# Optimization experiments

Hardware: AMD Instinct MI355X
Metric: run time of the kernel (lower is better)

Reference implementation:

```python
import jax, jax.numpy as jnp
import numpy as np

B, S, HID, HEADS, INTER = 64, 512, 40, 4, 20
DH = HID // HEADS  # 10
EPS = 1e-5


def layer_norm(x, g, b):
    mu = jnp.mean(x, axis=-1, keepdims=True)
    var = jnp.mean(jnp.square(x - mu), axis=-1, keepdims=True)
    return (x - mu) * jax.lax.rsqrt(var + EPS) * g + b


def setup_inputs() -> dict:
    key = jax.random.key(0)
    ks = jax.random.split(key, 16)
    s = 0.05
    return {
        "hidden_states": jax.random.normal(ks[0], (B, S, HID), jnp.float32),
        "ln1_g": jnp.ones((HID,), jnp.float32),
        "ln1_b": jnp.zeros((HID,), jnp.float32),
        "Wq": jax.random.normal(ks[1], (HID, HID), jnp.float32) * s,
        "bq": jnp.zeros((HID,), jnp.float32),
        "Wk": jax.random.normal(ks[2], (HID, HID), jnp.float32) * s,
        "bk": jnp.zeros((HID,), jnp.float32),
        "Wv": jax.random.normal(ks[3], (HID, HID), jnp.float32) * s,
        "bv": jnp.zeros((HID,), jnp.float32),
        "Wo": jax.random.normal(ks[4], (HID, HID), jnp.float32) * s,
        "bo": jnp.zeros((HID,), jnp.float32),
        "ln2_g": jnp.ones((HID,), jnp.float32),
        "ln2_b": jnp.zeros((HID,), jnp.float32),
        "W1": jax.random.normal(ks[5], (HID, INTER), jnp.float32) * s,
        "b1": jnp.zeros((INTER,), jnp.float32),
        "W2": jax.random.normal(ks[6], (INTER, HID), jnp.float32) * s,
        "b2": jnp.zeros((HID,), jnp.float32),
    }


def reference(hidden_states, ln1_g, ln1_b, Wq, bq, Wk, bk, Wv, bv, Wo, bo,
              ln2_g, ln2_b, W1, b1, W2, b2):
    x = hidden_states
    # --- self-attention (pre-LN) ---
    h = layer_norm(x, ln1_g, ln1_b)
    q = (h @ Wq + bq).reshape(B, S, HEADS, DH)
    k = (h @ Wk + bk).reshape(B, S, HEADS, DH)
    v = (h @ Wv + bv).reshape(B, S, HEADS, DH)
    # scores: [B, H, S, S]
    scores = jnp.einsum('bqhd,bkhd->bhqk', q, k) / jnp.sqrt(jnp.float32(DH))
    probs = jax.nn.softmax(scores, axis=-1)
    ctx = jnp.einsum('bhqk,bkhd->bqhd', probs, v).reshape(B, S, HID)
    attn_out = ctx @ Wo + bo + x
    # --- FFN (pre-LN) ---
    h2 = layer_norm(attn_out, ln2_g, ln2_b)
    inter = jax.nn.gelu(h2 @ W1 + b1, approximate=False)
    out = inter @ W2 + b2 + attn_out
    return out
```

## Files before the change

kernel.cpp:

```cpp
#include <hip/hip_runtime.h>
#include <stdint.h>

#define EPSF 1e-5f

typedef __attribute__((ext_vector_type(8)))  short bh8;
typedef __attribute__((ext_vector_type(16))) float fx16;
typedef __attribute__((ext_vector_type(4)))  int   i32x4;

__device__ __forceinline__ int cvtpk(float a, float b) {
    int r;
    asm("v_cvt_pk_bf16_f32 %0, %1, %2" : "=v"(r) : "v"(a), "v"(b));
    return r;
}
__device__ __forceinline__ float fastrcp(float x) {
    float r;
    asm("v_rcp_f32 %0, %1" : "=v"(r) : "v"(x));
    return r;
}

__global__ __launch_bounds__(512) void k_qkv_attn(
    const float* __restrict__ x, const float* __restrict__ g, const float* __restrict__ be,
    const float* __restrict__ Wq, const float* __restrict__ bq,
    const float* __restrict__ Wk, const float* __restrict__ bk,
    const float* __restrict__ Wv, const float* __restrict__ bv,
    float* __restrict__ ctx)
{
    __shared__ __align__(16) char smem[83968];

    const int tid = threadIdx.x;
    const int bh = blockIdx.x;
    const int b  = bh >> 2;
    const int h  = bh & 3;
    const int lane = tid & 63;
    const int wavei = tid >> 6;

    float* sX = (float*)smem;
    {
        const float4* xb = (const float4*)(x + (size_t)b * 512 * 40);
        for (int idx = tid; idx < 5120; idx += 512) {
            float4 u = xb[idx];
            int fl = idx * 4;
            int r = fl / 40, c = fl - r * 40;
            sX[r * 41 + c] = u.x; sX[r * 41 + c + 1] = u.y;
            sX[r * 41 + c + 2] = u.z; sX[r * 41 + c + 3] = u.w;
        }
    }
    __syncthreads();

    float s1 = 0.f, s2 = 0.f;
#pragma unroll 8
    for (int i = 0; i < 40; i++) { float v = sX[tid * 41 + i]; s1 += v; s2 += v * v; }
    const float mu = s1 * 0.025f;
    const float rs = rsqrtf(s2 * 0.025f - mu * mu + EPSF);

    float hrow[40];
#pragma unroll 4
    for (int i = 0; i < 40; i++)
        hrow[i] = (sX[tid * 41 + i] - mu) * rs * g[i] + be[i];

    float aq[10], ak[10], av[10];
#pragma unroll
    for (int c = 0; c < 10; c++) {
        aq[c] = bq[h * 10 + c]; ak[c] = bk[h * 10 + c]; av[c] = bv[h * 10 + c];
    }
#pragma unroll 2
    for (int i = 0; i < 40; i++) {
        const float hi = hrow[i];
        const float* wq = Wq + i * 40 + h * 10;
        const float* wk = Wk + i * 40 + h * 10;
        const float* wv = Wv + i * 40 + h * 10;
#pragma unroll
        for (int c = 0; c < 10; c++) {
            aq[c] += hi * wq[c]; ak[c] += hi * wk[c]; av[c] += hi * wv[c];
        }
    }
    const float cs = 1.4426950408889634f / 3.1622776601683795f;
#pragma unroll
    for (int c = 0; c < 10; c++) aq[c] *= cs;

    __syncthreads();

    char* sK  = smem;
    char* sVT = smem + 24576;
    char* sQ  = smem + 41216;
    {
        int p0 = cvtpk(ak[0], ak[1]), p1 = cvtpk(ak[2], ak[3]);
        int p2 = cvtpk(ak[4], ak[5]), p3 = cvtpk(ak[6], ak[7]);
        int p4 = cvtpk(ak[8], ak[9]);
        i32x4* kd = (i32x4*)(sK + tid * 48);
        kd[0] = (i32x4){p0, p1, p2, p3};
        kd[1] = (i32x4){p4, 0, 0, 0};
    }
    {
        int p0 = cvtpk(aq[0], aq[1]), p1 = cvtpk(aq[2], aq[3]);
        int p2 = cvtpk(aq[4], aq[5]), p3 = cvtpk(aq[6], aq[7]);
        int p4 = cvtpk(aq[8], aq[9]);
        i32x4* qd = (i32x4*)(sQ + tid * 32);
        qd[0] = (i32x4){p0, p1, p2, p3};
        qd[1] = (i32x4){p4, 0, 0, 0};
    }
    {
        int p0 = cvtpk(av[0], av[1]), p1 = cvtpk(av[2], av[3]);
        int p2 = cvtpk(av[4], av[5]), p3 = cvtpk(av[6], av[7]);
        int p4 = cvtpk(av[8], av[9]);
        unsigned short* vb = (unsigned short*)sVT + tid;
        vb[0 * 520] = (unsigned short)(p0 & 0xffff);
        vb[1 * 520] = (unsigned short)((unsigned)p0 >> 16);
        vb[2 * 520] = (unsigned short)(p1 & 0xffff);
        vb[3 * 520] = (unsigned short)((unsigned)p1 >> 16);
        vb[4 * 520] = (unsigned short)(p2 & 0xffff);
        vb[5 * 520] = (unsigned short)((unsigned)p2 >> 16);
        vb[6 * 520] = (unsigned short)(p3 & 0xffff);
        vb[7 * 520] = (unsigned short)((unsigned)p3 >> 16);
        vb[8 * 520] = (unsigned short)(p4 & 0xffff);
        vb[9 * 520] = (unsigned short)((unsigned)p4 >> 16);
        vb[10 * 520] = 0x3F80;
        vb[11 * 520] = 0; vb[12 * 520] = 0; vb[13 * 520] = 0;
        vb[14 * 520] = 0; vb[15 * 520] = 0;
    }
    __syncthreads();

    const int krow = lane & 31, khalf = lane >> 5;
    const int vrow = lane & 15;
    const bool vzero = (lane & 16) != 0;

    bh8 qf0 = *(const bh8*)(sQ + (size_t)(wavei * 64 + (lane & 31)) * 32 + (lane >> 5) * 16);
    bh8 qf1 = *(const bh8*)(sQ + (size_t)(wavei * 64 + 32 + (lane & 31)) * 32 + (lane >> 5) * 16);

    fx16 acc0 = (fx16)(0.0f), acc1 = (fx16)(0.0f);

    for (int kt = 0; kt < 16; ++kt) {
        bh8 kf  = *(const bh8*)(sK + (kt * 32 + krow) * 48 + khalf * 16);
        bh8 vf0 = *(const bh8*)(sVT + vrow * 1040 + kt * 64 + khalf * 16);
        bh8 vf1 = *(const bh8*)(sVT + vrow * 1040 + kt * 64 + 32 + khalf * 16);
        if (vzero) { vf0 = (bh8)(short)0; vf1 = (bh8)(short)0; }
#pragma unroll
        for (int qt = 0; qt < 2; ++qt) {
            fx16 s = __builtin_amdgcn_mfma_f32_32x32x16_bf16(
                kf, qt ? qf1 : qf0, (fx16)(0.0f), 0, 0, 0);
            float e[16];
#pragma unroll
            for (int r = 0; r < 16; ++r) e[r] = __builtin_amdgcn_exp2f(s[r]);
            int c0 = cvtpk(e[0], e[1]),   c1 = cvtpk(e[2], e[3]);
            int c2 = cvtpk(e[4], e[5]),   c3 = cvtpk(e[6], e[7]);
            int c4 = cvtpk(e[8], e[9]),   c5 = cvtpk(e[10], e[11]);
            int c6 = cvtpk(e[12], e[13]), c7 = cvtpk(e[14], e[15]);
            asm("v_permlane32_swap_b32 %0, %1" : "+v"(c0), "+v"(c2));
            asm("v_permlane32_swap_b32 %0, %1" : "+v"(c1), "+v"(c3));
            asm("v_permlane32_swap_b32 %0, %1" : "+v"(c4), "+v"(c6));
            asm("v_permlane32_swap_b32 %0, %1" : "+v"(c5), "+v"(c7));
            union { i32x4 i; bh8 h; } lo, hi;
            lo.i = (i32x4){c0, c1, c2, c3};
            hi.i = (i32x4){c4, c5, c6, c7};
            if (qt == 0) {
                acc0 = __builtin_amdgcn_mfma_f32_32x32x16_bf16(lo.h, vf0, acc0, 0, 0, 0);
                acc0 = __builtin_amdgcn_mfma_f32_32x32x16_bf16(hi.h, vf1, acc0, 0, 0, 0);
            } else {
                acc1 = __builtin_amdgcn_mfma_f32_32x32x16_bf16(lo.h, vf0, acc1, 0, 0, 0);
                acc1 = __builtin_amdgcn_mfma_f32_32x32x16_bf16(hi.h, vf1, acc1, 0, 0, 0);
            }
        }
    }

    const int d = lane & 31;
    const int qb = wavei * 64;
#pragma unroll
    for (int qt = 0; qt < 2; ++qt) {
        fx16 A = qt ? acc1 : acc0;
#pragma unroll
        for (int r = 0; r < 16; ++r) {
            float v = A[r];
            float ls = __shfl(v, (lane & 32) | 10, 64);
            float o = v * fastrcp(ls);
            if (d < 10) {
                int q = qb + qt * 32 + (r & 3) + 8 * (r >> 2) + 4 * (lane >> 5);
                ctx[((size_t)bh * 512 + q) * 10 + d] = o;
            }
        }
    }
}

__global__ __launch_bounds__(256) void k_out_ffn(
    const float* __restrict__ ctx, const float* __restrict__ x,
    const float* __restrict__ Wo, const float* __restrict__ bo,
    const float* __restrict__ g2, const float* __restrict__ bt2,
    const float* __restrict__ W1, const float* __restrict__ b1,
    const float* __restrict__ W2, const float* __restrict__ b2,
    float* __restrict__ out)
{
    __shared__ float sWo[40][48];
    __shared__ float sW1[40][32];
    __shared__ float sW2[20][48];
    __shared__ float sBo[40], sG2[40], sBt2[40], sB1[20], sB2[40];
    __shared__ float sCtx[64][41];
    __shared__ float sH[64][41];
    __shared__ float sIt[64][21];
    __shared__ float sSum[64][4], sSum2[64][4];

    const int tid = threadIdx.x;
    for (int idx = tid; idx < 1600; idx += 256) {
        int i = idx / 40, j = idx % 40;
        sWo[i][(j / 10) * 12 + (j % 10)] = Wo[idx];
    }
    for (int idx = tid; idx < 800; idx += 256) {
        {
            int i = idx / 20, j = idx % 20;
            sW1[i][(j / 5) * 8 + (j % 5)] = W1[idx];
        }
        {
            int i = idx / 40, j = idx % 40;
            sW2[i][(j / 10) * 12 + (j % 10)] = W2[idx];
        }
    }
    if (tid < 40) { sBo[tid] = bo[tid]; sG2[tid] = g2[tid]; sBt2[tid] = bt2[tid]; sB2[tid] = b2[tid]; }
    if (tid < 20) sB1[tid] = b1[tid];

    const int row0 = blockIdx.x * 64;
    const int b = row0 >> 9, s0 = row0 & 511;

    for (int idx = tid; idx < 640; idx += 256) {
        const int hh = idx / 160, f = idx - hh * 160;
        float4 u = *(const float4*)(ctx + ((size_t)((b * 4 + hh) * 512 + s0)) * 10 + f * 4);
        const int fo = f * 4;
        float e[4] = {u.x, u.y, u.z, u.w};
#pragma unroll
        for (int t = 0; t < 4; t++) {
            const int fe = fo + t;
            const int r = fe / 10, c = fe - r * 10;
            sCtx[r][hh * 10 + c] = e[t];
        }
    }
    const float4* xblk = (const float4*)(x + (size_t)blockIdx.x * 64 * 40);
    for (int idx = tid; idx < 640; idx += 256) {
        float4 w = xblk[idx];
        int fl = idx * 4;
        int r = fl / 40, c = fl - r * 40;
        sH[r][c] = w.x; sH[r][c + 1] = w.y; sH[r][c + 2] = w.z; sH[r][c + 3] = w.w;
    }
    __syncthreads();

    const int lane = tid & 63;
    const int wv = tid >> 6;
    const int j0 = wv * 10;

    float acc[10];
#pragma unroll
    for (int j = 0; j < 10; j++) acc[j] = sBo[j0 + j] + sH[lane][j0 + j];
#pragma unroll 8
    for (int i = 0; i < 40; i++) {
        const float ci = sCtx[lane][i];
        const float4* wrow = (const float4*)&sWo[i][wv * 12];
        float4 w0 = wrow[0], w1 = wrow[1], w2 = wrow[2];
        acc[0] += ci * w0.x; acc[1] += ci * w0.y; acc[2] += ci * w0.z; acc[3] += ci * w0.w;
        acc[4] += ci * w1.x; acc[5] += ci * w1.y; acc[6] += ci * w1.z; acc[7] += ci * w1.w;
        acc[8] += ci * w2.x; acc[9] += ci * w2.y;
    }
    {
        float s1 = 0.f, s2 = 0.f;
#pragma unroll
        for (int j = 0; j < 10; j++) { s1 += acc[j]; s2 += acc[j] * acc[j]; }
        sSum[lane][wv] = s1; sSum2[lane][wv] = s2;
    }
    __syncthreads();
    const float mu = (sSum[lane][0] + sSum[lane][1] + sSum[lane][2] + sSum[lane][3]) * 0.025f;
    const float ex2 = (sSum2[lane][0] + sSum2[lane][1] + sSum2[lane][2] + sSum2[lane][3]) * 0.025f;
    const float rs = rsqrtf(ex2 - mu * mu + EPSF);
#pragma unroll
    for (int j = 0; j < 10; j++)
        sH[lane][j0 + j] = (acc[j] - mu) * rs * sG2[j0 + j] + sBt2[j0 + j];
    __syncthreads();

    const int f0 = wv * 5;
    float it[5];
#pragma unroll
    for (int j = 0; j < 5; j++) it[j] = sB1[f0 + j];
#pragma unroll 8
    for (int i = 0; i < 40; i++) {
        const float hi = sH[lane][i];
        const float4* wrow = (const float4*)&sW1[i][wv * 8];
        float4 w0 = wrow[0], w1 = wrow[1];
        it[0] += hi * w0.x; it[1] += hi * w0.y; it[2] += hi * w0.z; it[3] += hi * w0.w;
        it[4] += hi * w1.x;
    }
#pragma unroll
    for (int j = 0; j < 5; j++) {
        float t = it[j];
        sIt[lane][f0 + j] = 0.5f * t * (1.0f + erff(t * 0.70710678118654752f));
    }
    __syncthreads();

    float o[10];
#pragma unroll
    for (int j = 0; j < 10; j++) o[j] = acc[j] + sB2[j0 + j];
#pragma unroll 4
    for (int i = 0; i < 20; i++) {
        const float ii = sIt[lane][i];
        const float4* wrow = (const float4*)&sW2[i][wv * 12];
        float4 w0 = wrow[0], w1 = wrow[1], w2 = wrow[2];
        o[0] += ii * w0.x; o[1] += ii * w0.y; o[2] += ii * w0.z; o[3] += ii * w0.w;
        o[4] += ii * w1.x; o[5] += ii * w1.y; o[6] += ii * w1.z; o[7] += ii * w1.w;
        o[8] += ii * w2.x; o[9] += ii * w2.y;
    }
#pragma unroll
    for (int j = 0; j < 10; j++) sCtx[lane][j0 + j] = o[j];
    __syncthreads();

    float4* oblk = (float4*)(out + (size_t)blockIdx.x * 64 * 40);
    for (int idx = tid; idx < 640; idx += 256) {
        int fl = idx * 4;
        int r = fl / 40, c = fl - r * 40;
        float4 u;
        u.x = sCtx[r][c]; u.y = sCtx[r][c + 1]; u.z = sCtx[r][c + 2]; u.w = sCtx[r][c + 3];
        oblk[idx] = u;
    }
}

extern "C" void kernel_launch(void* const* d_in, const int* in_sizes, int n_in,
                              void* d_out, int out_size, void* d_ws, size_t ws_size,
                              hipStream_t stream)
{
    const float* x   = (const float*)d_in[0];
    const float* g1  = (const float*)d_in[1];
    const float* be1 = (const float*)d_in[2];
    const float* Wq  = (const float*)d_in[3];
    const float* bq  = (const float*)d_in[4];
    const float* Wk  = (const float*)d_in[5];
    const float* bk  = (const float*)d_in[6];
    const float* Wv  = (const float*)d_in[7];
    const float* bv  = (const float*)d_in[8];
    const float* Wo  = (const float*)d_in[9];
    const float* bo  = (const float*)d_in[10];
    const float* g2  = (const float*)d_in[11];
    const float* bt2 = (const float*)d_in[12];
    const float* W1  = (const float*)d_in[13];
    const float* b1  = (const float*)d_in[14];
    const float* W2  = (const float*)d_in[15];
    const float* b2  = (const float*)d_in[16];

    float* ctx = (float*)d_ws;

    k_qkv_attn<<<256, 512, 0, stream>>>(x, g1, be1, Wq, bq, Wk, bk, Wv, bv, ctx);
    k_out_ffn<<<512, 256, 0, stream>>>(ctx, x, Wo, bo, g2, bt2, W1, b1, W2, b2,
                                       (float*)d_out);
}
```

Measured before the change: 129.3 us.

## Store ctx token-major and compute out-proj/FFN per row in one wave

The attention kernel now writes context in [B,S,HID] layout with heads interleaved, so the second kernel can load it with contiguous float4 reads. The out-projection/LN2/FFN kernel is reshaped from 4 waves splitting columns to a single 64-thread wave where each thread owns a full row. This removes the cross-wave LayerNorm reduction, several barriers and the shared-memory weight staging; weights are read directly from global memory as uniform loads. The cost is high register pressure (40+40+20 accumulators per thread) and much lower occupancy per block, since only 512 single-wave blocks are launched.

New measurement: 152.5 us. +18.0%, slower.

```diff
diff --git a/kernel.cpp b/kernel.cpp
--- a/kernel.cpp
+++ b/kernel.cpp
@@ -174,13 +174,13 @@
             float o = v * fastrcp(ls);
             if (d < 10) {
                 int q = qb + qt * 32 + (r & 3) + 8 * (r >> 2) + 4 * (lane >> 5);
-                ctx[((size_t)bh * 512 + q) * 10 + d] = o;
+                ctx[((size_t)b * 512 + q) * 40 + h * 10 + d] = o;
             }
         }
     }
 }
 
-__global__ __launch_bounds__(256) void k_out_ffn(
+__global__ __launch_bounds__(64) void k_out_ffn(
     const float* __restrict__ ctx, const float* __restrict__ x,
     const float* __restrict__ Wo, const float* __restrict__ bo,
     const float* __restrict__ g2, const float* __restrict__ bt2,
@@ -188,129 +188,81 @@
     const float* __restrict__ W2, const float* __restrict__ b2,
     float* __restrict__ out)
 {
-    __shared__ float sWo[40][48];
-    __shared__ float sW1[40][32];
-    __shared__ float sW2[20][48];
-    __shared__ float sBo[40], sG2[40], sBt2[40], sB1[20], sB2[40];
-    __shared__ float sCtx[64][41];
-    __shared__ float sH[64][41];
-    __shared__ float sIt[64][21];
-    __shared__ float sSum[64][4], sSum2[64][4];
+    __shared__ float sX[64][41];
+    __shared__ float sC[64][41];
 
     const int tid = threadIdx.x;
-    for (int idx = tid; idx < 1600; idx += 256) {
-        int i = idx / 40, j = idx % 40;
-        sWo[i][(j / 10) * 12 + (j % 10)] = Wo[idx];
-    }
-    for (int idx = tid; idx < 800; idx += 256) {
-        {
-            int i = idx / 20, j = idx % 20;
-            sW1[i][(j / 5) * 8 + (j % 5)] = W1[idx];
-        }
-        {
-            int i = idx / 40, j = idx % 40;
-            sW2[i][(j / 10) * 12 + (j % 10)] = W2[idx];
-        }
-    }
-    if (tid < 40) { sBo[tid] = bo[tid]; sG2[tid] = g2[tid]; sBt2[tid] = bt2[tid]; sB2[tid] = b2[tid]; }
-    if (tid < 20) sB1[tid] = b1[tid];
-
-    const int row0 = blockIdx.x * 64;
-    const int b = row0 >> 9, s0 = row0 & 511;
-
-    for (int idx = tid; idx < 640; idx += 256) {
-        const int hh = idx / 160, f = idx - hh * 160;
-        float4 u = *(const float4*)(ctx + ((size_t)((b * 4 + hh) * 512 + s0)) * 10 + f * 4);
-        const int fo = f * 4;
-        float e[4] = {u.x, u.y, u.z, u.w};
-#pragma unroll
-        for (int t = 0; t < 4; t++) {
-            const int fe = fo + t;
-            const int r = fe / 10, c = fe - r * 10;
-            sCtx[r][hh * 10 + c] = e[t];
-        }
-    }
     const float4* xblk = (const float4*)(x + (size_t)blockIdx.x * 64 * 40);
-    for (int idx = tid; idx < 640; idx += 256) {
-        float4 w = xblk[idx];
+    const float4* cblk = (const float4*)(ctx + (size_t)blockIdx.x * 64 * 40);
+    for (int idx = tid; idx < 640; idx += 64) {
+        float4 u = xblk[idx];
+        float4 v = cblk[idx];
         int fl = idx * 4;
         int r = fl / 40, c = fl - r * 40;
-        sH[r][c] = w.x; sH[r][c + 1] = w.y; sH[r][c + 2] = w.z; sH[r][c + 3] = w.w;
-    }
-    __syncthreads();
-
-    const int lane = tid & 63;
-    const int wv = tid >> 6;
-    const int j0 = wv * 10;
-
-    float acc[10];
-#pragma unroll
-    for (int j = 0; j < 10; j++) acc[j] = sBo[j0 + j] + sH[lane][j0 + j];
-#pragma unroll 8
+        sX[r][c] = u.x; sX[r][c + 1] = u.y; sX[r][c + 2] = u.z; sX[r][c + 3] = u.w;
+        sC[r][c] = v.x; sC[r][c + 1] = v.y; sC[r][c + 2] = v.z; sC[r][c + 3] = v.w;
+    }
+    __syncthreads();
+
+    float acc[40];
+#pragma unroll 8
+    for (int c = 0; c < 40; c++) acc[c] = sX[tid][c] + bo[c];
+#pragma unroll 2
     for (int i = 0; i < 40; i++) {
-        const float ci = sCtx[lane][i];
-        const float4* wrow = (const float4*)&sWo[i][wv * 12];
-        float4 w0 = wrow[0], w1 = wrow[1], w2 = wrow[2];
-        acc[0] += ci * w0.x; acc[1] += ci * w0.y; acc[2] += ci * w0.z; acc[3] += ci * w0.w;
-        acc[4] += ci * w1.x; acc[5] += ci * w1.y; acc[6] += ci * w1.z; acc[7] += ci * w1.w;
-        acc[8] += ci * w2.x; acc[9] += ci * w2.y;
-    }
-    {
-        float s1 = 0.f, s2 = 0.f;
-#pragma unroll
-        for (int j = 0; j < 10; j++) { s1 += acc[j]; s2 += acc[j] * acc[j]; }
-        sSum[lane][wv] = s1; sSum2[lane][wv] = s2;
-    }
-    __syncthreads();
-    const float mu = (sSum[lane][0] + sSum[lane][1] + sSum[lane][2] + sSum[lane][3]) * 0.025f;
-    const float ex2 = (sSum2[lane][0] + sSum2[lane][1] + sSum2[lane][2] + sSum2[lane][3]) * 0.025f;
-    const float rs = rsqrtf(ex2 - mu * mu + EPSF);
-#pragma unroll
-    for (int j = 0; j < 10; j++)
-        sH[lane][j0 + j] = (acc[j] - mu) * rs * sG2[j0 + j] + sBt2[j0 + j];
-    __syncthreads();
-
-    const int f0 = wv * 5;
-    float it[5];
-#pragma unroll
-    for (int j = 0; j < 5; j++) it[j] = sB1[f0 + j];
-#pragma unroll 8
+        const float ci = sC[tid][i];
+        const float* wp = Wo + i * 40;
+#pragma unroll
+        for (int c = 0; c < 40; c++) acc[c] += ci * wp[c];
+    }
+
+    float s1 = 0.f, s2 = 0.f;
+#pragma unroll 8
+    for (int c = 0; c < 40; c++) { s1 += acc[c]; s2 += acc[c] * acc[c]; }
+    const float mu = s1 * 0.025f;
+    const float rs = rsqrtf(s2 * 0.025f - mu * mu + EPSF);
+
+    float h2[40];
+#pragma unroll 4
+    for (int c = 0; c < 40; c++)
+        h2[c] = (acc[c] - mu) * rs * g2[c] + bt2[c];
+
+    float it[20];
+#pragma unroll
+    for (int j = 0; j < 20; j++) it[j] = b1[j];
+#pragma unroll 2
     for (int i = 0; i < 40; i++) {
-        const float hi = sH[lane][i];
-        const float4* wrow = (const float4*)&sW1[i][wv * 8];
-        float4 w0 = wrow[0], w1 = wrow[1];
-        it[0] += hi * w0.x; it[1] += hi * w0.y; it[2] += hi * w0.z; it[3] += hi * w0.w;
-        it[4] += hi * w1.x;
-    }
-#pragma unroll
-    for (int j = 0; j < 5; j++) {
+        const float hi = h2[i];
+        const float* wp = W1 + i * 20;
+#pragma unroll
+        for (int j = 0; j < 20; j++) it[j] += hi * wp[j];
+    }
+#pragma unroll 4
+    for (int j = 0; j < 20; j++) {
         float t = it[j];
-        sIt[lane][f0 + j] = 0.5f * t * (1.0f + erff(t * 0.70710678118654752f));
-    }
-    __syncthreads();
-
-    float o[10];
-#pragma unroll
-    for (int j = 0; j < 10; j++) o[j] = acc[j] + sB2[j0 + j];
-#pragma unroll 4
+        it[j] = 0.5f * t * (1.0f + erff(t * 0.70710678118654752f));
+    }
+
+#pragma unroll 8
+    for (int c = 0; c < 40; c++) acc[c] += b2[c];
+#pragma unroll 2
     for (int i = 0; i < 20; i++) {
-        const float ii = sIt[lane][i];
-        const float4* wrow = (const float4*)&sW2[i][wv * 12];
-        float4 w0 = wrow[0], w1 = wrow[1], w2 = wrow[2];
-        o[0] += ii * w0.x; o[1] += ii * w0.y; o[2] += ii * w0.z; o[3] += ii * w0.w;
-        o[4] += ii * w1.x; o[5] += ii * w1.y; o[6] += ii * w1.z; o[7] += ii * w1.w;
-        o[8] += ii * w2.x; o[9] += ii * w2.y;
-    }
-#pragma unroll
-    for (int j = 0; j < 10; j++) sCtx[lane][j0 + j] = o[j];
+        const float ii = it[i];
+        const float* wp = W2 + i * 40;
+#pragma unroll
+        for (int c = 0; c < 40; c++) acc[c] += ii * wp[c];
+    }
+
+    __syncthreads();
+#pragma unroll 8
+    for (int c = 0; c < 40; c++) sC[tid][c] = acc[c];
     __syncthreads();
 
     float4* oblk = (float4*)(out + (size_t)blockIdx.x * 64 * 40);
-    for (int idx = tid; idx < 640; idx += 256) {
+    for (int idx = tid; idx < 640; idx += 64) {
         int fl = idx * 4;
         int r = fl / 40, c = fl - r * 40;
         float4 u;
-        u.x = sCtx[r][c]; u.y = sCtx[r][c + 1]; u.z = sCtx[r][c + 2]; u.w = sCtx[r][c + 3];
+        u.x = sC[r][c]; u.y = sC[r][c + 1]; u.z = sC[r][c + 2]; u.w = sC[r][c + 3];
         oblk[idx] = u;
     }
 }
@@ -340,6 +292,6 @@
     float* ctx = (float*)d_ws;
 
     k_qkv_attn<<<256, 512, 0, stream>>>(x, g1, be1, Wq, bq, Wk, bk, Wv, bv, ctx);
-    k_out_ffn<<<512, 256, 0, stream>>>(ctx, x, Wo, bo, g2, bt2, W1, b1, W2, b2,
-                                       (float*)d_out);
-}
+    k_out_ffn<<<512, 64, 0, stream>>>(ctx, x, Wo, bo, g2, bt2, W1, b1, W2, b2,
+                                      (float*)d_out);
+}
```
